# Kernel tuning notes

Measured on AMD Instinct MI355X. Metric: run time of the kernel, lower is better.

## Reference

```python
import jax, jax.numpy as jnp
import numpy as np

N = 50000
E = 800000
IN_C = 128
HID = 64
HEADS = 4
NEG_SLOPE = 0.2
EPS = 1e-16


def setup_inputs() -> dict:
    key = jax.random.key(0)
    ks = jax.random.split(key, 12)
    x = jax.random.normal(ks[0], (N, IN_C), dtype=jnp.float32)
    edge_index = jax.random.randint(ks[1], (2, E), 0, N, dtype=jnp.int64)
    # layer 1: in -> (HEADS, HID), concat heads
    W1 = jax.random.normal(ks[2], (IN_C, HEADS * HID), dtype=jnp.float32) * (1.0 / np.sqrt(IN_C))
    a_src1 = jax.random.normal(ks[3], (HEADS, HID), dtype=jnp.float32) * 0.1
    a_dst1 = jax.random.normal(ks[4], (HEADS, HID), dtype=jnp.float32) * 0.1
    b1 = jnp.zeros((HEADS * HID,), dtype=jnp.float32)
    # layer 2: HEADS*HID -> (1, HID)
    W2 = jax.random.normal(ks[5], (HEADS * HID, HID), dtype=jnp.float32) * (1.0 / np.sqrt(HEADS * HID))
    a_src2 = jax.random.normal(ks[6], (1, HID), dtype=jnp.float32) * 0.1
    a_dst2 = jax.random.normal(ks[7], (1, HID), dtype=jnp.float32) * 0.1
    b2 = jnp.zeros((HID,), dtype=jnp.float32)
    return {"x": x, "edge_index": edge_index, "W1": W1, "a_src1": a_src1,
            "a_dst1": a_dst1, "b1": b1, "W2": W2, "a_src2": a_src2,
            "a_dst2": a_dst2, "b2": b2}


def _gat_conv(x, src, dst, W, a_src, a_dst, bias, heads, ch):
    n = x.shape[0]
    h = (x @ W).reshape(n, heads, ch)                       # [N,H,C]
    alpha_s = jnp.einsum('nhc,hc->nh', h, a_src)            # [N,H]
    alpha_d = jnp.einsum('nhc,hc->nh', h, a_dst)            # [N,H]
    e = jax.nn.leaky_relu(alpha_s[src] + alpha_d[dst], NEG_SLOPE)  # [E,H]
    # segment softmax over incoming edges of each dst node
    m = jax.ops.segment_max(e, dst, num_segments=n)         # [N,H]
    ex = jnp.exp(e - m[dst])
    denom = jax.ops.segment_sum(ex, dst, num_segments=n)    # [N,H]
    alpha = ex / (denom[dst] + EPS)                         # [E,H]
    msg = h[src] * alpha[:, :, None]                        # [E,H,C]
    out = jax.ops.segment_sum(msg, dst, num_segments=n)     # [N,H,C]
    return out.reshape(n, heads * ch) + bias


def reference(x, edge_index, W1, a_src1, a_dst1, b1, W2, a_src2, a_dst2, b2):
    src = edge_index[0]
    dst = edge_index[1]
    h = _gat_conv(x, src, dst, W1, a_src1, a_dst1, b1, HEADS, HID)
    h = jax.nn.elu(h)
    h = _gat_conv(h, src, dst, W2, a_src2, a_dst2, b2, 1, HID)
    h = jax.nn.elu(h)
    return h  # [N, HID] (output_dim == hidden_channels so no final linear)
```

## Files before the change

### kernel.cpp

```cpp
#include <hip/hip_runtime.h>
#include <math.h>

#define NN 50000
#define EE 800000
#define IN_C 128
#define HID 64
#define HEADS 4
#define SCAN_BLOCKS ((NN + 255) / 256)
#define EBLOCKS ((EE + 255) / 256)

typedef __attribute__((ext_vector_type(8))) short bf16x8;
typedef __attribute__((ext_vector_type(4))) float f32x4;


__device__ inline unsigned short f2bf(float f) {
    unsigned u = __float_as_uint(f);
    return (unsigned short)((u + 0x7fff + ((u >> 16) & 1)) >> 16);
}
__device__ inline float bf2f(unsigned short s) {
    return __uint_as_float(((unsigned)s) << 16);
}

__device__ inline int wave_incl_scan(int v, int lane) {
    #pragma unroll
    for (int off = 1; off < 64; off <<= 1) {
        int t = __shfl_up(v, off);
        if (lane >= off) v += t;
    }
    return v;
}

__device__ inline int block256_excl_scan(int v, int tid, int* ws4) {
    int lane = tid & 63, wv = tid >> 6;
    int incl = wave_incl_scan(v, lane);
    if (lane == 63) ws4[wv] = incl;
    __syncthreads();
    if (tid == 0) {
        int run = 0;
        #pragma unroll
        for (int i = 0; i < 4; i++) { int t = ws4[i]; ws4[i] = run; run += t; }
    }
    __syncthreads();
    return incl + ws4[wv] - v;
}


__global__ void prep_kernel(const int* __restrict__ ei, int* __restrict__ deg,
                            const float* __restrict__ W1, unsigned short* __restrict__ W1Thi,
                            unsigned short* __restrict__ W1Tlo,
                            const float* __restrict__ W2, unsigned short* __restrict__ W2Thi,
                            unsigned short* __restrict__ W2Tlo) {
    int b = blockIdx.x;
    int tid = threadIdx.x;
    if (b < EBLOCKS) {
        int i = b * 256 + tid;
        if (i < EE) atomicAdd(&deg[ei[EE + i]], 1);
    } else if (b < EBLOCKS + 128) {
        int idx = (b - EBLOCKS) * 256 + tid;
        int r = idx >> 8, c = idx & 255;
        float v = W1[idx];
        unsigned short h = f2bf(v);
        W1Thi[c * 128 + r] = h;
        W1Tlo[c * 128 + r] = f2bf(v - bf2f(h));
    } else {
        int idx = (b - EBLOCKS - 128) * 256 + tid;
        int r = idx >> 6, c = idx & 63;
        float v = W2[idx];
        unsigned short h = f2bf(v);
        W2Thi[c * 256 + r] = h;
        W2Tlo[c * 256 + r] = f2bf(v - bf2f(h));
    }
}


__global__ void deg_partial_kernel(const int* __restrict__ deg, int* __restrict__ bsum) {
    __shared__ int ws4[4];
    int tid = threadIdx.x;
    int idx = blockIdx.x * 256 + tid;
    int d = (idx < NN) ? deg[idx] : 0;
    int lane = tid & 63, wv = tid >> 6;
    int s = d;
    #pragma unroll
    for (int off = 32; off; off >>= 1) s += __shfl_down(s, off);
    if (lane == 0) ws4[wv] = s;
    __syncthreads();
    if (tid == 0) bsum[blockIdx.x] = ws4[0] + ws4[1] + ws4[2] + ws4[3];
}

__global__ void scanb_kernel(const int* __restrict__ bsum, int* __restrict__ boff,
                             int* __restrict__ row_ptr) {
    __shared__ int ws4[4];
    int tid = threadIdx.x;
    int v = (tid < SCAN_BLOCKS) ? bsum[tid] : 0;
    int excl = block256_excl_scan(v, tid, ws4);
    if (tid < SCAN_BLOCKS) boff[tid] = excl;
    if (tid == 255) row_ptr[NN] = excl + v;
}

__global__ void fill_kernel(const int* __restrict__ deg, const int* __restrict__ boff,
                            int* __restrict__ row_ptr, int* __restrict__ cursor) {
    __shared__ int ws4[4];
    int tid = threadIdx.x;
    int idx = blockIdx.x * 256 + tid;
    int d = (idx < NN) ? deg[idx] : 0;
    int excl = block256_excl_scan(d, tid, ws4) + boff[blockIdx.x];
    if (idx < NN) { row_ptr[idx] = excl; cursor[idx] = excl; }
}

__global__ void scatter_kernel(const int* __restrict__ ei, int* __restrict__ cursor,
                               int* __restrict__ csr_src) {
    int i = blockIdx.x * blockDim.x + threadIdx.x;
    if (i < EE) {
        int d = ei[EE + i];
        int pos = atomicAdd(&cursor[d], 1);
        csr_src[pos] = ei[i];
    }
}

__global__ __launch_bounds__(256) void gemm1_mfma(
        const float* __restrict__ x,
        const unsigned short* __restrict__ Bhi, const unsigned short* __restrict__ Blo,
        const float* __restrict__ a_src, const float* __restrict__ a_dst,
        unsigned short* __restrict__ h1b, float* __restrict__ as1, float* __restrict__ ad1) {
    __shared__ unsigned short Ahi[32][136];
    __shared__ unsigned short Alo[32][136];
    int tid = threadIdx.x;
    int w = tid >> 6, lane = tid & 63;
    int lq = lane >> 4, lr = lane & 15;
    int brow = blockIdx.x * 32;
    {
        int row = tid >> 3;
        int col0 = (tid & 7) * 16;
        int gr = min(brow + row, NN - 1);
        #pragma unroll
        for (int i = 0; i < 16; i += 4) {
            float4 v = *(const float4*)(x + (size_t)gr * 128 + col0 + i);
            unsigned short h0 = f2bf(v.x), h1 = f2bf(v.y), h2 = f2bf(v.z), h3 = f2bf(v.w);
            Ahi[row][col0 + i + 0] = h0; Alo[row][col0 + i + 0] = f2bf(v.x - bf2f(h0));
            Ahi[row][col0 + i + 1] = h1; Alo[row][col0 + i + 1] = f2bf(v.y - bf2f(h1));
            Ahi[row][col0 + i + 2] = h2; Alo[row][col0 + i + 2] = f2bf(v.z - bf2f(h2));
            Ahi[row][col0 + i + 3] = h3; Alo[row][col0 + i + 3] = f2bf(v.w - bf2f(h3));
        }
    }
    __syncthreads();
    f32x4 acc[2][4];
    f32x4 zf = {0.f, 0.f, 0.f, 0.f};
    #pragma unroll
    for (int mi = 0; mi < 2; mi++)
        #pragma unroll
        for (int ni = 0; ni < 4; ni++) acc[mi][ni] = zf;
    #pragma unroll
    for (int q = 0; q < 4; q++) {
        int ko = q * 32 + lq * 8;
        bf16x8 ah0 = *(const bf16x8*)(const void*)&Ahi[lr][ko];
        bf16x8 al0 = *(const bf16x8*)(const void*)&Alo[lr][ko];
        bf16x8 ah1 = *(const bf16x8*)(const void*)&Ahi[16 + lr][ko];
        bf16x8 al1 = *(const bf16x8*)(const void*)&Alo[16 + lr][ko];
        #pragma unroll
        for (int ni = 0; ni < 4; ni++) {
            size_t bo = (size_t)(w * 64 + ni * 16 + lr) * 128 + ko;
            bf16x8 bh = *(const bf16x8*)(const void*)(Bhi + bo);
            bf16x8 bl = *(const bf16x8*)(const void*)(Blo + bo);
            acc[0][ni] = __builtin_amdgcn_mfma_f32_16x16x32_bf16(al0, bh, acc[0][ni], 0, 0, 0);
            acc[0][ni] = __builtin_amdgcn_mfma_f32_16x16x32_bf16(ah0, bl, acc[0][ni], 0, 0, 0);
            acc[0][ni] = __builtin_amdgcn_mfma_f32_16x16x32_bf16(ah0, bh, acc[0][ni], 0, 0, 0);
            acc[1][ni] = __builtin_amdgcn_mfma_f32_16x16x32_bf16(al1, bh, acc[1][ni], 0, 0, 0);
            acc[1][ni] = __builtin_amdgcn_mfma_f32_16x16x32_bf16(ah1, bl, acc[1][ni], 0, 0, 0);
            acc[1][ni] = __builtin_amdgcn_mfma_f32_16x16x32_bf16(ah1, bh, acc[1][ni], 0, 0, 0);
        }
    }
    float asv[4], adv[4];
    #pragma unroll
    for (int ni = 0; ni < 4; ni++) {
        asv[ni] = a_src[w * 64 + ni * 16 + lr];
        adv[ni] = a_dst[w * 64 + ni * 16 + lr];
    }
    #pragma unroll
    for (int mi = 0; mi < 2; mi++) {
        f32x4 ps = zf, pd = zf;
        #pragma unroll
        for (int ni = 0; ni < 4; ni++)
            #pragma unroll
            for (int r = 0; r < 4; r++) {
                ps[r] += acc[mi][ni][r] * asv[ni];
                pd[r] += acc[mi][ni][r] * adv[ni];
            }
        #pragma unroll
        for (int m = 1; m < 16; m <<= 1)
            #pragma unroll
            for (int r = 0; r < 4; r++) {
                ps[r] += __shfl_xor(ps[r], m);
                pd[r] += __shfl_xor(pd[r], m);
            }
        #pragma unroll
        for (int r = 0; r < 4; r++) {
            int n = brow + mi * 16 + lq * 4 + r;
            if (lr == 0 && n < NN) { as1[n * 4 + w] = ps[r]; ad1[n * 4 + w] = pd[r]; }
        }
        #pragma unroll
        for (int ni = 0; ni < 4; ni++)
            #pragma unroll
            for (int r = 0; r < 4; r++) {
                int n = brow + mi * 16 + lq * 4 + r;
                if (n < NN)
                    h1b[(size_t)n * 256 + w * 64 + ni * 16 + lr] = f2bf(acc[mi][ni][r]);
            }
    }
}

__global__ __launch_bounds__(256) void gemm2_mfma(
        const unsigned short* __restrict__ Ahi, const unsigned short* __restrict__ Alo,
        const unsigned short* __restrict__ Bhi, const unsigned short* __restrict__ Blo,
        const float* __restrict__ a_src, const float* __restrict__ a_dst,
        unsigned short* __restrict__ g2b, float* __restrict__ as2, float* __restrict__ ad2) {
    int tid = threadIdx.x;
    int w = tid >> 6, lane = tid & 63;
    int lq = lane >> 4, lr = lane & 15;
    int wrow = blockIdx.x * 128 + w * 32;
    f32x4 acc[2][4];
    f32x4 zf = {0.f, 0.f, 0.f, 0.f};
    #pragma unroll
    for (int mi = 0; mi < 2; mi++)
        #pragma unroll
        for (int ni = 0; ni < 4; ni++) acc[mi][ni] = zf;
    int ra = min(wrow + lr, NN - 1);
    int rb = min(wrow + 16 + lr, NN - 1);
    #pragma unroll
    for (int q = 0; q < 8; q++) {
        int ko = q * 32 + lq * 8;
        bf16x8 ah0 = *(const bf16x8*)(const void*)(Ahi + (size_t)ra * 256 + ko);
        bf16x8 al0 = *(const bf16x8*)(const void*)(Alo + (size_t)ra * 256 + ko);
        bf16x8 ah1 = *(const bf16x8*)(const void*)(Ahi + (size_t)rb * 256 + ko);
        bf16x8 al1 = *(const bf16x8*)(const void*)(Alo + (size_t)rb * 256 + ko);
        #pragma unroll
        for (int ni = 0; ni < 4; ni++) {
            size_t bo = (size_t)(ni * 16 + lr) * 256 + ko;
            bf16x8 bh = *(const bf16x8*)(const void*)(Bhi + bo);
            bf16x8 bl = *(const bf16x8*)(const void*)(Blo + bo);
            acc[0][ni] = __builtin_amdgcn_mfma_f32_16x16x32_bf16(al0, bh, acc[0][ni], 0, 0, 0);
            acc[0][ni] = __builtin_amdgcn_mfma_f32_16x16x32_bf16(ah0, bl, acc[0][ni], 0, 0, 0);
            acc[0][ni] = __builtin_amdgcn_mfma_f32_16x16x32_bf16(ah0, bh, acc[0][ni], 0, 0, 0);
            acc[1][ni] = __builtin_amdgcn_mfma_f32_16x16x32_bf16(al1, bh, acc[1][ni], 0, 0, 0);
            acc[1][ni] = __builtin_amdgcn_mfma_f32_16x16x32_bf16(ah1, bl, acc[1][ni], 0, 0, 0);
            acc[1][ni] = __builtin_amdgcn_mfma_f32_16x16x32_bf16(ah1, bh, acc[1][ni], 0, 0, 0);
        }
    }
    float asv[4], adv[4];
    #pragma unroll
    for (int ni = 0; ni < 4; ni++) {
        asv[ni] = a_src[ni * 16 + lr];
        adv[ni] = a_dst[ni * 16 + lr];
    }
    #pragma unroll
    for (int mi = 0; mi < 2; mi++) {
        f32x4 ps = zf, pd = zf;
        #pragma unroll
        for (int ni = 0; ni < 4; ni++)
            #pragma unroll
            for (int r = 0; r < 4; r++) {
                ps[r] += acc[mi][ni][r] * asv[ni];
                pd[r] += acc[mi][ni][r] * adv[ni];
            }
        #pragma unroll
        for (int m = 1; m < 16; m <<= 1)
            #pragma unroll
            for (int r = 0; r < 4; r++) {
                ps[r] += __shfl_xor(ps[r], m);
                pd[r] += __shfl_xor(pd[r], m);
            }
        #pragma unroll
        for (int r = 0; r < 4; r++) {
            int n = wrow + mi * 16 + lq * 4 + r;
            if (lr == 0 && n < NN) { as2[n] = ps[r]; ad2[n] = pd[r]; }
        }
        #pragma unroll
        for (int ni = 0; ni < 4; ni++)
            #pragma unroll
            for (int r = 0; r < 4; r++) {
                int n = wrow + mi * 16 + lq * 4 + r;
                if (n < NN)
                    g2b[(size_t)n * 64 + ni * 16 + lr] = f2bf(acc[mi][ni][r]);
            }
    }
}

__global__ __launch_bounds__(256) void agg1_kernel(
        const unsigned short* __restrict__ h1b, const int* __restrict__ row_ptr,
        const int* __restrict__ csr_src, const float* __restrict__ as,
        const float* __restrict__ ad, const float* __restrict__ b1,
        unsigned short* __restrict__ h2hi, unsigned short* __restrict__ h2lo) {
    __shared__ int   ssrc[4][64];
    __shared__ float wch[4][64][4];
    int tid = threadIdx.x;
    int wv = tid >> 6, lane = tid & 63;
    int n = blockIdx.x * 4 + wv;
    if (n >= NN) return;
    int start = row_ptr[n], end = row_ptr[n + 1];
    float4 adv = ((const float4*)ad)[n];
    int whead = lane >> 4;
    float4 acc = make_float4(0.f, 0.f, 0.f, 0.f);
    float d0 = 0.f, d1 = 0.f, d2 = 0.f, d3 = 0.f;
    for (int c0 = start; c0 < end; c0 += 64) {
        int m = min(64, end - c0);
        if (lane < m) {
            int s = csr_src[c0 + lane];
            ssrc[wv][lane] = s;
            float4 asv = ((const float4*)as)[s];
            float e0 = asv.x + adv.x; e0 = e0 > 0.f ? e0 : 0.2f * e0; float x0 = __expf(e0);
            float e1 = asv.y + adv.y; e1 = e1 > 0.f ? e1 : 0.2f * e1; float x1 = __expf(e1);
            float e2 = asv.z + adv.z; e2 = e2 > 0.f ? e2 : 0.2f * e2; float x2 = __expf(e2);
            float e3 = asv.w + adv.w; e3 = e3 > 0.f ? e3 : 0.2f * e3; float x3 = __expf(e3);
            *(float4*)&wch[wv][lane][0] = make_float4(x0, x1, x2, x3);
            d0 += x0; d1 += x1; d2 += x2; d3 += x3;
        }
        int j = 0;
        for (; j + 4 <= m; j += 4) {
            int   sj[4]; float wj[4]; ushort4 hv[4];
            #pragma unroll
            for (int u = 0; u < 4; u++) {
                sj[u] = ssrc[wv][j + u];
                wj[u] = wch[wv][j + u][whead];
            }
            #pragma unroll
            for (int u = 0; u < 4; u++)
                hv[u] = ((const ushort4*)h1b)[(size_t)sj[u] * 64 + lane];
            #pragma unroll
            for (int u = 0; u < 4; u++) {
                acc.x += bf2f(hv[u].x) * wj[u]; acc.y += bf2f(hv[u].y) * wj[u];
                acc.z += bf2f(hv[u].z) * wj[u]; acc.w += bf2f(hv[u].w) * wj[u];
            }
        }
        for (; j < m; j++) {
            int s = ssrc[wv][j];
            float w = wch[wv][j][whead];
            ushort4 hv = ((const ushort4*)h1b)[(size_t)s * 64 + lane];
            acc.x += bf2f(hv.x) * w; acc.y += bf2f(hv.y) * w;
            acc.z += bf2f(hv.z) * w; acc.w += bf2f(hv.w) * w;
        }
    }
    #pragma unroll
    for (int off = 32; off; off >>= 1) {
        d0 += __shfl_down(d0, off); d1 += __shfl_down(d1, off);
        d2 += __shfl_down(d2, off); d3 += __shfl_down(d3, off);
    }
    d0 = __shfl(d0, 0); d1 = __shfl(d1, 0);
    d2 = __shfl(d2, 0); d3 = __shfl(d3, 0);
    float den = whead == 0 ? d0 : whead == 1 ? d1 : whead == 2 ? d2 : d3;
    float inv = 1.f / (den + 1e-16f);
    float4 bv = ((const float4*)b1)[lane];
    float4 r;
    r.x = acc.x * inv + bv.x; r.y = acc.y * inv + bv.y;
    r.z = acc.z * inv + bv.z; r.w = acc.w * inv + bv.w;
    r.x = r.x > 0.f ? r.x : expm1f(r.x);
    r.y = r.y > 0.f ? r.y : expm1f(r.y);
    r.z = r.z > 0.f ? r.z : expm1f(r.z);
    r.w = r.w > 0.f ? r.w : expm1f(r.w);
    ushort4 hi4, lo4;
    hi4.x = f2bf(r.x); lo4.x = f2bf(r.x - bf2f(hi4.x));
    hi4.y = f2bf(r.y); lo4.y = f2bf(r.y - bf2f(hi4.y));
    hi4.z = f2bf(r.z); lo4.z = f2bf(r.z - bf2f(hi4.z));
    hi4.w = f2bf(r.w); lo4.w = f2bf(r.w - bf2f(hi4.w));
    ((ushort4*)h2hi)[(size_t)n * 64 + lane] = hi4;
    ((ushort4*)h2lo)[(size_t)n * 64 + lane] = lo4;
}

__global__ __launch_bounds__(256) void agg2_kernel(
        const unsigned short* __restrict__ g2b, const int* __restrict__ row_ptr,
        const int* __restrict__ csr_src, const float* __restrict__ as,
        const float* __restrict__ ad, const float* __restrict__ b2,
        float* __restrict__ out) {
    __shared__ int   ssrc[4][64];
    __shared__ float wts[4][64];
    int tid = threadIdx.x;
    int wv = tid >> 6, lane = tid & 63;
    int n = blockIdx.x * 4 + wv;
    if (n >= NN) return;
    int start = row_ptr[n], end = row_ptr[n + 1];
    float adv = ad[n];
    float acc = 0.f;
    float den = 0.f;
    for (int c0 = start; c0 < end; c0 += 64) {
        int m = min(64, end - c0);
        if (lane < m) {
            int s = csr_src[c0 + lane];
            ssrc[wv][lane] = s;
            float e = as[s] + adv;
            e = e > 0.f ? e : 0.2f * e;
            float x = __expf(e);
            wts[wv][lane] = x;
            den += x;
        }
        int j = 0;
        for (; j + 4 <= m; j += 4) {
            int sj[4]; float wj[4]; unsigned short gv[4];
            #pragma unroll
            for (int u = 0; u < 4; u++) {
                sj[u] = ssrc[wv][j + u];
                wj[u] = wts[wv][j + u];
            }
            #pragma unroll
            for (int u = 0; u < 4; u++)
                gv[u] = g2b[(size_t)sj[u] * 64 + lane];
            #pragma unroll
            for (int u = 0; u < 4; u++)
                acc += bf2f(gv[u]) * wj[u];
        }
        for (; j < m; j++) {
            int s = ssrc[wv][j];
            acc += bf2f(g2b[(size_t)s * 64 + lane]) * wts[wv][j];
        }
    }
    #pragma unroll
    for (int off = 32; off; off >>= 1) den += __shfl_down(den, off);
    den = __shfl(den, 0);
    float inv = 1.f / (den + 1e-16f);
    float r = acc * inv + b2[lane];
    out[(size_t)n * 64 + lane] = r > 0.f ? r : expm1f(r);
}


extern "C" void kernel_launch(void* const* d_in, const int* in_sizes, int n_in,
                              void* d_out, int out_size, void* d_ws, size_t ws_size,
                              hipStream_t stream) {
    const float* x      = (const float*)d_in[0];
    const int*   ei     = (const int*)d_in[1];
    const float* W1     = (const float*)d_in[2];
    const float* a_src1 = (const float*)d_in[3];
    const float* a_dst1 = (const float*)d_in[4];
    const float* b1     = (const float*)d_in[5];
    const float* W2     = (const float*)d_in[6];
    const float* a_src2 = (const float*)d_in[7];
    const float* a_dst2 = (const float*)d_in[8];
    const float* b2     = (const float*)d_in[9];
    float* out = (float*)d_out;

    char* base = (char*)d_ws;
    size_t off = 0;
    auto alloc = [&](size_t bytes) -> void* {
        void* p = base + off;
        off = (off + bytes + 255) & ~(size_t)255;
        return p;
    };
    int*   deg     = (int*)alloc(NN * sizeof(int));
    int*   bsum    = (int*)alloc(SCAN_BLOCKS * sizeof(int));
    int*   boff    = (int*)alloc(SCAN_BLOCKS * sizeof(int));
    int*   row_ptr = (int*)alloc((NN + 1) * sizeof(int));
    int*   cursor  = (int*)alloc(NN * sizeof(int));
    int*   csr_src = (int*)alloc(EE * sizeof(int));
    unsigned short* W1Thi = (unsigned short*)alloc(256 * 128 * 2);
    unsigned short* W1Tlo = (unsigned short*)alloc(256 * 128 * 2);
    unsigned short* W2Thi = (unsigned short*)alloc(64 * 256 * 2);
    unsigned short* W2Tlo = (unsigned short*)alloc(64 * 256 * 2);
    unsigned short* h1b   = (unsigned short*)alloc((size_t)NN * 256 * 2);
    float* as1     = (float*)alloc((size_t)NN * 4 * sizeof(float));
    float* ad1     = (float*)alloc((size_t)NN * 4 * sizeof(float));
    unsigned short* h2hi  = (unsigned short*)alloc((size_t)NN * 256 * 2);
    unsigned short* h2lo  = (unsigned short*)alloc((size_t)NN * 256 * 2);
    unsigned short* g2b   = (unsigned short*)alloc((size_t)NN * 64 * 2);
    float* as2     = (float*)alloc((size_t)NN * sizeof(float));
    float* ad2     = (float*)alloc((size_t)NN * sizeof(float));

    hipMemsetAsync(deg, 0, NN * sizeof(int), stream);

    prep_kernel<<<EBLOCKS + 128 + 64, 256, 0, stream>>>(ei, deg, W1, W1Thi, W1Tlo,
                                                        W2, W2Thi, W2Tlo);
    deg_partial_kernel<<<SCAN_BLOCKS, 256, 0, stream>>>(deg, bsum);
    scanb_kernel<<<1, 256, 0, stream>>>(bsum, boff, row_ptr);
    fill_kernel<<<SCAN_BLOCKS, 256, 0, stream>>>(deg, boff, row_ptr, cursor);
    scatter_kernel<<<EBLOCKS, 256, 0, stream>>>(ei, cursor, csr_src);

    gemm1_mfma<<<(NN + 31) / 32, 256, 0, stream>>>(x, W1Thi, W1Tlo,
                                                   a_src1, a_dst1, h1b, as1, ad1);
    agg1_kernel<<<(NN + 3) / 4, 256, 0, stream>>>(h1b, row_ptr, csr_src, as1, ad1, b1,
                                                  h2hi, h2lo);

    gemm2_mfma<<<(NN + 127) / 128, 256, 0, stream>>>(h2hi, h2lo, W2Thi, W2Tlo,
                                                     a_src2, a_dst2, g2b, as2, ad2);
    agg2_kernel<<<(NN + 3) / 4, 256, 0, stream>>>(g2b, row_ptr, csr_src, as2, ad2, b2, out);
}
```

Baseline: 330.8 us.

## Fuse edge scatter into gemm1 launch and use bf16 dot2 in aggregations

```diff
diff --git a/kernel.cpp b/kernel.cpp
--- a/kernel.cpp
+++ b/kernel.cpp
@@ -8,9 +8,16 @@
 #define HEADS 4
 #define SCAN_BLOCKS ((NN + 255) / 256)
 #define EBLOCKS ((EE + 255) / 256)
+#define GEMM1B ((NN + 31) / 32)
 
 typedef __attribute__((ext_vector_type(8))) short bf16x8;
 typedef __attribute__((ext_vector_type(4))) float f32x4;
+
+#if defined(__has_builtin)
+#if __has_builtin(__builtin_amdgcn_fdot2_f32_bf16)
+#define HAVE_FDOT2_BF16 1
+#endif
+#endif
 
 
 __device__ inline unsigned short f2bf(float f) {
@@ -20,6 +27,21 @@
 __device__ inline float bf2f(unsigned short s) {
     return __uint_as_float(((unsigned)s) << 16);
 }
+__device__ inline unsigned prm(unsigned a, unsigned b, unsigned sel) {
+    return __builtin_amdgcn_perm(a, b, sel);
+}
+#ifdef HAVE_FDOT2_BF16
+typedef __attribute__((ext_vector_type(2))) __bf16 bf2v;
+__device__ inline float fdot2bf(unsigned h, unsigned w, float acc) {
+    return __builtin_amdgcn_fdot2_f32_bf16(__builtin_bit_cast(bf2v, h),
+                                           __builtin_bit_cast(bf2v, w), acc, false);
+}
+#else
+__device__ inline float fdot2bf(unsigned h, unsigned w, float acc) {
+    return acc + bf2f((unsigned short)(h & 0xffff)) * bf2f((unsigned short)(w & 0xffff))
+               + bf2f((unsigned short)(h >> 16)) * bf2f((unsigned short)(w >> 16));
+}
+#endif
 
 __device__ inline int wave_incl_scan(int v, int lane) {
     #pragma unroll
@@ -45,11 +67,11 @@
 }
 
 
-__global__ void prep_kernel(const int* __restrict__ ei, int* __restrict__ deg,
-                            const float* __restrict__ W1, unsigned short* __restrict__ W1Thi,
-                            unsigned short* __restrict__ W1Tlo,
-                            const float* __restrict__ W2, unsigned short* __restrict__ W2Thi,
-                            unsigned short* __restrict__ W2Tlo) {
+__global__ void front_kernel(const int* __restrict__ ei, int* __restrict__ deg,
+                             const float* __restrict__ W1, unsigned short* __restrict__ W1Thi,
+                             unsigned short* __restrict__ W1Tlo,
+                             const float* __restrict__ W2, unsigned short* __restrict__ W2Thi,
+                             unsigned short* __restrict__ W2Tlo) {
     int b = blockIdx.x;
     int tid = threadIdx.x;
     if (b < EBLOCKS) {
@@ -107,17 +129,8 @@
     if (idx < NN) { row_ptr[idx] = excl; cursor[idx] = excl; }
 }
 
-__global__ void scatter_kernel(const int* __restrict__ ei, int* __restrict__ cursor,
-                               int* __restrict__ csr_src) {
-    int i = blockIdx.x * blockDim.x + threadIdx.x;
-    if (i < EE) {
-        int d = ei[EE + i];
-        int pos = atomicAdd(&cursor[d], 1);
-        csr_src[pos] = ei[i];
-    }
-}
-
-__global__ __launch_bounds__(256) void gemm1_mfma(
+__global__ __launch_bounds__(256) void scatter_gemm1_kernel(
+        const int* __restrict__ ei, int* __restrict__ cursor, int* __restrict__ csr_src,
         const float* __restrict__ x,
         const unsigned short* __restrict__ Bhi, const unsigned short* __restrict__ Blo,
         const float* __restrict__ a_src, const float* __restrict__ a_dst,
@@ -125,9 +138,18 @@
     __shared__ unsigned short Ahi[32][136];
     __shared__ unsigned short Alo[32][136];
     int tid = threadIdx.x;
+    if (blockIdx.x < EBLOCKS) {
+        int i = blockIdx.x * 256 + tid;
+        if (i < EE) {
+            int d = ei[EE + i];
+            int pos = atomicAdd(&cursor[d], 1);
+            csr_src[pos] = ei[i];
+        }
+        return;
+    }
     int w = tid >> 6, lane = tid & 63;
     int lq = lane >> 4, lr = lane & 15;
-    int brow = blockIdx.x * 32;
+    int brow = (blockIdx.x - EBLOCKS) * 32;
     {
         int row = tid >> 3;
         int col0 = (tid & 7) * 16;
@@ -289,8 +311,8 @@
         const int* __restrict__ csr_src, const float* __restrict__ as,
         const float* __restrict__ ad, const float* __restrict__ b1,
         unsigned short* __restrict__ h2hi, unsigned short* __restrict__ h2lo) {
-    __shared__ int   ssrc[4][64];
-    __shared__ float wch[4][64][4];
+    __shared__ int            ssrc[4][64];
+    __shared__ unsigned short wbf[4][4][64];
     int tid = threadIdx.x;
     int wv = tid >> 6, lane = tid & 63;
     int n = blockIdx.x * 4 + wv;
@@ -310,29 +332,44 @@
             float e1 = asv.y + adv.y; e1 = e1 > 0.f ? e1 : 0.2f * e1; float x1 = __expf(e1);
             float e2 = asv.z + adv.z; e2 = e2 > 0.f ? e2 : 0.2f * e2; float x2 = __expf(e2);
             float e3 = asv.w + adv.w; e3 = e3 > 0.f ? e3 : 0.2f * e3; float x3 = __expf(e3);
-            *(float4*)&wch[wv][lane][0] = make_float4(x0, x1, x2, x3);
+            wbf[wv][0][lane] = f2bf(x0);
+            wbf[wv][1][lane] = f2bf(x1);
+            wbf[wv][2][lane] = f2bf(x2);
+            wbf[wv][3][lane] = f2bf(x3);
             d0 += x0; d1 += x1; d2 += x2; d3 += x3;
         }
         int j = 0;
         for (; j + 4 <= m; j += 4) {
-            int   sj[4]; float wj[4]; ushort4 hv[4];
-            #pragma unroll
-            for (int u = 0; u < 4; u++) {
-                sj[u] = ssrc[wv][j + u];
-                wj[u] = wch[wv][j + u][whead];
-            }
-            #pragma unroll
-            for (int u = 0; u < 4; u++)
-                hv[u] = ((const ushort4*)h1b)[(size_t)sj[u] * 64 + lane];
-            #pragma unroll
-            for (int u = 0; u < 4; u++) {
-                acc.x += bf2f(hv[u].x) * wj[u]; acc.y += bf2f(hv[u].y) * wj[u];
-                acc.z += bf2f(hv[u].z) * wj[u]; acc.w += bf2f(hv[u].w) * wj[u];
-            }
-        }
-        for (; j < m; j++) {
+            int s0 = ssrc[wv][j], s1 = ssrc[wv][j + 1];
+            int s2 = ssrc[wv][j + 2], s3 = ssrc[wv][j + 3];
+            uint2 ha = ((const uint2*)h1b)[(size_t)s0 * 64 + lane];
+            uint2 hb = ((const uint2*)h1b)[(size_t)s1 * 64 + lane];
+            uint2 hc = ((const uint2*)h1b)[(size_t)s2 * 64 + lane];
+            uint2 hd = ((const uint2*)h1b)[(size_t)s3 * 64 + lane];
+            unsigned wp01 = *(const unsigned*)&wbf[wv][whead][j];
+            unsigned wp23 = *(const unsigned*)&wbf[wv][whead][j + 2];
+            acc.x = fdot2bf(prm(hb.x, ha.x, 0x05040100), wp01, acc.x);
+            acc.y = fdot2bf(prm(hb.x, ha.x, 0x07060302), wp01, acc.y);
+            acc.z = fdot2bf(prm(hb.y, ha.y, 0x05040100), wp01, acc.z);
+            acc.w = fdot2bf(prm(hb.y, ha.y, 0x07060302), wp01, acc.w);
+            acc.x = fdot2bf(prm(hd.x, hc.x, 0x05040100), wp23, acc.x);
+            acc.y = fdot2bf(prm(hd.x, hc.x, 0x07060302), wp23, acc.y);
+            acc.z = fdot2bf(prm(hd.y, hc.y, 0x05040100), wp23, acc.z);
+            acc.w = fdot2bf(prm(hd.y, hc.y, 0x07060302), wp23, acc.w);
+        }
+        for (; j + 2 <= m; j += 2) {
+            int s0 = ssrc[wv][j], s1 = ssrc[wv][j + 1];
+            uint2 ha = ((const uint2*)h1b)[(size_t)s0 * 64 + lane];
+            uint2 hb = ((const uint2*)h1b)[(size_t)s1 * 64 + lane];
+            unsigned wp = *(const unsigned*)&wbf[wv][whead][j];
+            acc.x = fdot2bf(prm(hb.x, ha.x, 0x05040100), wp, acc.x);
+            acc.y = fdot2bf(prm(hb.x, ha.x, 0x07060302), wp, acc.y);
+            acc.z = fdot2bf(prm(hb.y, ha.y, 0x05040100), wp, acc.z);
+            acc.w = fdot2bf(prm(hb.y, ha.y, 0x07060302), wp, acc.w);
+        }
+        if (j < m) {
             int s = ssrc[wv][j];
-            float w = wch[wv][j][whead];
+            float w = bf2f(wbf[wv][whead][j]);
             ushort4 hv = ((const ushort4*)h1b)[(size_t)s * 64 + lane];
             acc.x += bf2f(hv.x) * w; acc.y += bf2f(hv.y) * w;
             acc.z += bf2f(hv.z) * w; acc.w += bf2f(hv.w) * w;
@@ -369,8 +406,8 @@
         const int* __restrict__ csr_src, const float* __restrict__ as,
         const float* __restrict__ ad, const float* __restrict__ b2,
         float* __restrict__ out) {
-    __shared__ int   ssrc[4][64];
-    __shared__ float wts[4][64];
+    __shared__ int            ssrc[4][64];
+    __shared__ unsigned short wbf[4][64];
     int tid = threadIdx.x;
     int wv = tid >> 6, lane = tid & 63;
     int n = blockIdx.x * 4 + wv;
@@ -387,27 +424,32 @@
             float e = as[s] + adv;
             e = e > 0.f ? e : 0.2f * e;
             float x = __expf(e);
-            wts[wv][lane] = x;
+            wbf[wv][lane] = f2bf(x);
             den += x;
         }
         int j = 0;
         for (; j + 4 <= m; j += 4) {
-            int sj[4]; float wj[4]; unsigned short gv[4];
-            #pragma unroll
-            for (int u = 0; u < 4; u++) {
-                sj[u] = ssrc[wv][j + u];
-                wj[u] = wts[wv][j + u];
-            }
-            #pragma unroll
-            for (int u = 0; u < 4; u++)
-                gv[u] = g2b[(size_t)sj[u] * 64 + lane];
-            #pragma unroll
-            for (int u = 0; u < 4; u++)
-                acc += bf2f(gv[u]) * wj[u];
-        }
-        for (; j < m; j++) {
+            int s0 = ssrc[wv][j], s1 = ssrc[wv][j + 1];
+            int s2 = ssrc[wv][j + 2], s3 = ssrc[wv][j + 3];
+            unsigned g0 = g2b[(size_t)s0 * 64 + lane];
+            unsigned g1 = g2b[(size_t)s1 * 64 + lane];
+            unsigned g2 = g2b[(size_t)s2 * 64 + lane];
+            unsigned g3 = g2b[(size_t)s3 * 64 + lane];
+            unsigned wp01 = *(const unsigned*)&wbf[wv][j];
+            unsigned wp23 = *(const unsigned*)&wbf[wv][j + 2];
+            acc = fdot2bf(prm(g1, g0, 0x05040100), wp01, acc);
+            acc = fdot2bf(prm(g3, g2, 0x05040100), wp23, acc);
+        }
+        for (; j + 2 <= m; j += 2) {
+            int s0 = ssrc[wv][j], s1 = ssrc[wv][j + 1];
+            unsigned g0 = g2b[(size_t)s0 * 64 + lane];
+            unsigned g1 = g2b[(size_t)s1 * 64 + lane];
+            unsigned wp = *(const unsigned*)&wbf[wv][j];
+            acc = fdot2bf(prm(g1, g0, 0x05040100), wp, acc);
+        }
+        if (j < m) {
             int s = ssrc[wv][j];
-            acc += bf2f(g2b[(size_t)s * 64 + lane]) * wts[wv][j];
+            acc += bf2f(g2b[(size_t)s * 64 + lane]) * bf2f(wbf[wv][j]);
         }
     }
     #pragma unroll
@@ -462,18 +504,17 @@
 
     hipMemsetAsync(deg, 0, NN * sizeof(int), stream);
 
-    prep_kernel<<<EBLOCKS + 128 + 64, 256, 0, stream>>>(ei, deg, W1, W1Thi, W1Tlo,
-                                                        W2, W2Thi, W2Tlo);
+    front_kernel<<<EBLOCKS + 128 + 64, 256, 0, stream>>>(ei, deg, W1, W1Thi, W1Tlo,
+                                                         W2, W2Thi, W2Tlo);
     deg_partial_kernel<<<SCAN_BLOCKS, 256, 0, stream>>>(deg, bsum);
     scanb_kernel<<<1, 256, 0, stream>>>(bsum, boff, row_ptr);
     fill_kernel<<<SCAN_BLOCKS, 256, 0, stream>>>(deg, boff, row_ptr, cursor);
-    scatter_kernel<<<EBLOCKS, 256, 0, stream>>>(ei, cursor, csr_src);
-
-    gemm1_mfma<<<(NN + 31) / 32, 256, 0, stream>>>(x, W1Thi, W1Tlo,
-                                                   a_src1, a_dst1, h1b, as1, ad1);
+
+    scatter_gemm1_kernel<<<EBLOCKS + GEMM1B, 256, 0, stream>>>(
+        ei, cursor, csr_src, x, W1Thi, W1Tlo, a_src1, a_dst1, h1b, as1, ad1);
+
     agg1_kernel<<<(NN + 3) / 4, 256, 0, stream>>>(h1b, row_ptr, csr_src, as1, ad1, b1,
                                                   h2hi, h2lo);
-
     gemm2_mfma<<<(NN + 127) / 128, 256, 0, stream>>>(h2hi, h2lo, W2Thi, W2Tlo,
                                                      a_src2, a_dst2, g2b, as2, ad2);
     agg2_kernel<<<(NN + 3) / 4, 256, 0, stream>>>(g2b, row_ptr, csr_src, as2, ad2, b2, out);
```

New measurement: 342.5 us. 3.5% more time.
